# Optimization experiments

Measured on AMD Instinct MI355X. Metric: run time of the kernel, lower is better.

Reference implementation:

```python
import jax, jax.numpy as jnp
import numpy as np

NUM_BINS = 22
TEMPLATE_DIM = 16
MAX_DIST = 40.0
LN_EPS = 1e-5


def setup_inputs() -> dict:
    key = jax.random.key(0)
    k1, k2, k3, k4, k5, k6 = jax.random.split(key, 6)
    B, N = 2, 1024
    template_coords = jax.random.normal(k1, (B, N, 3), dtype=jnp.float32) * 10.0  # Angstrom-ish scale
    confidence = jax.random.uniform(k2, (B, N), dtype=jnp.float32)
    # projection = Linear(22 -> 16) + LayerNorm(16)
    lim = 1.0 / np.sqrt(NUM_BINS)
    W = jax.random.uniform(k3, (NUM_BINS, TEMPLATE_DIM), minval=-lim, maxval=lim, dtype=jnp.float32)
    b = jax.random.uniform(k4, (TEMPLATE_DIM,), minval=-lim, maxval=lim, dtype=jnp.float32)
    gamma = jnp.ones((TEMPLATE_DIM,), dtype=jnp.float32)
    beta = jnp.zeros((TEMPLATE_DIM,), dtype=jnp.float32)
    return {"template_coords": template_coords, "confidence": confidence,
            "W": W, "b": b, "gamma": gamma, "beta": beta}


def reference(template_coords, confidence, W, b, gamma, beta):
    num_dist_bins = NUM_BINS - 1          # 21
    bin_width = MAX_DIST / num_dist_bins
    bin_edges = jnp.arange(0.0, MAX_DIST, bin_width, dtype=jnp.float32)  # (21,)
    no_template_bin = NUM_BINS - 1

    # pairwise distances (B, N, N)
    diff = template_coords[:, :, None, :] - template_coords[:, None, :, :]
    dist = jnp.sqrt(jnp.sum(diff * diff, axis=-1) + 1e-8)

    # torch.bucketize(right=False) == searchsorted side='left'
    binned = jnp.searchsorted(bin_edges, dist, side="left")
    binned = jnp.clip(binned, 0, NUM_BINS - 2)

    has_i = (confidence > 0)[:, :, None]
    has_j = (confidence > 0)[:, None, :]
    binned = jnp.where(has_i & has_j, binned, no_template_bin)

    one_hot = jax.nn.one_hot(binned, NUM_BINS, dtype=jnp.float32)  # (B,N,N,22)

    # Linear + LayerNorm + ReLU
    h = jnp.einsum("bijk,kd->bijd", one_hot, W) + b
    mu = jnp.mean(h, axis=-1, keepdims=True)
    var = jnp.mean((h - mu) ** 2, axis=-1, keepdims=True)
    h = (h - mu) * jax.lax.rsqrt(var + LN_EPS) * gamma + beta
    h = jax.nn.relu(h)

    conf_pair = jnp.minimum(confidence[:, :, None], confidence[:, None, :])
    return h * conf_pair[..., None]
```

## Files before the change

### kernel.cpp

```cpp
#include <hip/hip_runtime.h>

#define BATCH 2
#define N 1024
#define NBINS 22
#define TDIM 16
#define TSTR 20

__global__ __launch_bounds__(256) void te_enc(
    const float* __restrict__ coords,
    const float* __restrict__ confp,
    const float* __restrict__ Wp,
    const float* __restrict__ bp,
    const float* __restrict__ gp,
    const float* __restrict__ betap,
    float* __restrict__ out)
{
    __shared__ __align__(16) float tbl[NBINS * TSTR];
    __shared__ float4 ljc[N];

    const int tid = threadIdx.x;
    const int blk = blockIdx.x;
    const int batch = blk >> 10;
    const int i = blk & (N - 1);

    const float* jc = coords + batch * N * 3;
    const float* jf = confp + batch * N;

    #pragma unroll
    for (int q = 0; q < 4; ++q) {
        const int j = tid + q * 256;
        float4 v;
        v.x = jc[j * 3 + 0];
        v.y = jc[j * 3 + 1];
        v.z = jc[j * 3 + 2];
        v.w = jf[j];
        ljc[j] = v;
    }

    if (tid < NBINS) {
        float h[TDIM];
        float sum = 0.f;
        #pragma unroll
        for (int d = 0; d < TDIM; ++d) {
            h[d] = Wp[tid * TDIM + d] + bp[d];
            sum += h[d];
        }
        const float mu = sum * (1.f / TDIM);
        float s2 = 0.f;
        #pragma unroll
        for (int d = 0; d < TDIM; ++d) {
            const float t = h[d] - mu;
            s2 += t * t;
        }
        const float rs = 1.f / sqrtf(s2 * (1.f / TDIM) + 1e-5f);
        #pragma unroll
        for (int d = 0; d < TDIM; ++d) {
            const float v = (h[d] - mu) * rs * gp[d] + betap[d];
            tbl[tid * TSTR + d] = fmaxf(v, 0.f);
        }
    }
    __syncthreads();

    const float xi = coords[(batch * N + i) * 3 + 0];
    const float yi = coords[(batch * N + i) * 3 + 1];
    const float zi = coords[(batch * N + i) * 3 + 2];
    const float ci = confp[batch * N + i];
    const bool ci_ok = (ci > 0.f);

    const int w   = tid >> 6;
    const int l   = tid & 63;
    const int lq  = l >> 2;
    const int sub = l & 3;

    float4* orow4 = (float4*)out + ((size_t)(batch * N + i)) * (N * TDIM / 4);
    const float EW = (float)(40.0 / 21.0);

    #pragma unroll
    for (int it = 0; it < 4; ++it) {
        const int j_base = it * 256 + w * 64;
        #pragma unroll
        for (int c = 0; c < 4; ++c) {
            const int j = j_base + 16 * c + lq;
            const float4 pj = ljc[j];

            const float dx = __fsub_rn(xi, pj.x);
            const float dy = __fsub_rn(yi, pj.y);
            const float dz = __fsub_rn(zi, pj.z);
            float s = __fmul_rn(dx, dx);
            s = __fadd_rn(s, __fmul_rn(dy, dy));
            s = __fadd_rn(s, __fmul_rn(dz, dz));
            s = __fadd_rn(s, 1e-8f);
            const float dist = __fsqrt_rn(s);

            int k0 = (int)__fmul_rn(dist, 0.525f);
            k0 = k0 < 20 ? k0 : 20;
            const int c1 = (__fmul_rn((float)k0, EW) < dist) ? 1 : 0;
            const int c2 = (__fmul_rn((float)(k0 + 1), EW) < dist) ? 1 : 0;
            const int idx = k0 + c1 + c2;
            int bin = idx < 20 ? idx : 20;
            if (!(ci_ok && pj.w > 0.f)) bin = NBINS - 1;
            const float cm = fminf(ci, pj.w);

            const float4 r = *(const float4*)&tbl[bin * TSTR + sub * 4];
            float4 o;
            o.x = r.x * cm; o.y = r.y * cm; o.z = r.z * cm; o.w = r.w * cm;

            orow4[j_base * 4 + 64 * c + l] = o;
        }
    }
}

extern "C" void kernel_launch(void* const* d_in, const int* in_sizes, int n_in,
                              void* d_out, int out_size, void* d_ws, size_t ws_size,
                              hipStream_t stream) {
    const float* coords = (const float*)d_in[0];
    const float* conf   = (const float*)d_in[1];
    const float* W      = (const float*)d_in[2];
    const float* b      = (const float*)d_in[3];
    const float* g      = (const float*)d_in[4];
    const float* beta   = (const float*)d_in[5];
    float* out          = (float*)d_out;

    te_enc<<<dim3(BATCH * N), dim3(256), 0, stream>>>(coords, conf, W, b, g, beta, out);
}
```

Baseline: 145.6 us.

## Split each row across four blocks and use nontemporal output stores

Each block now handles a quarter of the j range for one row i, giving four times as many blocks, each staging only 256 coordinates in shared memory. Output writes use nontemporal stores through a native vector type so the large streaming output bypasses cache retention. The cost is that the per-block LayerNorm table setup and the i-coordinate loads are repeated four times as often.

```diff
diff --git a/kernel.cpp b/kernel.cpp
--- a/kernel.cpp
+++ b/kernel.cpp
@@ -5,6 +5,9 @@
 #define NBINS 22
 #define TDIM 16
 #define TSTR 20
+#define SEGS 4
+
+typedef float nfloat4 __attribute__((ext_vector_type(4)));
 
 __global__ __launch_bounds__(256) void te_enc(
     const float* __restrict__ coords,
@@ -16,25 +19,25 @@
     float* __restrict__ out)
 {
     __shared__ __align__(16) float tbl[NBINS * TSTR];
-    __shared__ float4 ljc[N];
+    __shared__ float4 ljc[N / SEGS];
 
     const int tid = threadIdx.x;
     const int blk = blockIdx.x;
-    const int batch = blk >> 10;
-    const int i = blk & (N - 1);
+    const int batch = blk >> 12;
+    const int i   = (blk >> 2) & (N - 1);
+    const int seg = blk & (SEGS - 1);
 
     const float* jc = coords + batch * N * 3;
     const float* jf = confp + batch * N;
 
-    #pragma unroll
-    for (int q = 0; q < 4; ++q) {
-        const int j = tid + q * 256;
+    {
+        const int j = seg * 256 + tid;
         float4 v;
         v.x = jc[j * 3 + 0];
         v.y = jc[j * 3 + 1];
         v.z = jc[j * 3 + 2];
         v.w = jf[j];
-        ljc[j] = v;
+        ljc[tid] = v;
     }
 
     if (tid < NBINS) {
@@ -72,41 +75,38 @@
     const int lq  = l >> 2;
     const int sub = l & 3;
 
-    float4* orow4 = (float4*)out + ((size_t)(batch * N + i)) * (N * TDIM / 4);
+    nfloat4* orow4 = (nfloat4*)out + ((size_t)(batch * N + i)) * (N * TDIM / 4)
+                   + seg * 1024 + w * 256;
     const float EW = (float)(40.0 / 21.0);
 
     #pragma unroll
-    for (int it = 0; it < 4; ++it) {
-        const int j_base = it * 256 + w * 64;
-        #pragma unroll
-        for (int c = 0; c < 4; ++c) {
-            const int j = j_base + 16 * c + lq;
-            const float4 pj = ljc[j];
+    for (int c = 0; c < 4; ++c) {
+        const int jl = w * 64 + 16 * c + lq;
+        const float4 pj = ljc[jl];
 
-            const float dx = __fsub_rn(xi, pj.x);
-            const float dy = __fsub_rn(yi, pj.y);
-            const float dz = __fsub_rn(zi, pj.z);
-            float s = __fmul_rn(dx, dx);
-            s = __fadd_rn(s, __fmul_rn(dy, dy));
-            s = __fadd_rn(s, __fmul_rn(dz, dz));
-            s = __fadd_rn(s, 1e-8f);
-            const float dist = __fsqrt_rn(s);
+        const float dx = __fsub_rn(xi, pj.x);
+        const float dy = __fsub_rn(yi, pj.y);
+        const float dz = __fsub_rn(zi, pj.z);
+        float s = __fmul_rn(dx, dx);
+        s = __fadd_rn(s, __fmul_rn(dy, dy));
+        s = __fadd_rn(s, __fmul_rn(dz, dz));
+        s = __fadd_rn(s, 1e-8f);
+        const float dist = __fsqrt_rn(s);
 
-            int k0 = (int)__fmul_rn(dist, 0.525f);
-            k0 = k0 < 20 ? k0 : 20;
-            const int c1 = (__fmul_rn((float)k0, EW) < dist) ? 1 : 0;
-            const int c2 = (__fmul_rn((float)(k0 + 1), EW) < dist) ? 1 : 0;
-            const int idx = k0 + c1 + c2;
-            int bin = idx < 20 ? idx : 20;
-            if (!(ci_ok && pj.w > 0.f)) bin = NBINS - 1;
-            const float cm = fminf(ci, pj.w);
+        int k0 = (int)__fmul_rn(dist, 0.525f);
+        k0 = k0 < 20 ? k0 : 20;
+        const int c1 = (__fmul_rn((float)k0, EW) < dist) ? 1 : 0;
+        const int c2 = (__fmul_rn((float)(k0 + 1), EW) < dist) ? 1 : 0;
+        const int idx = k0 + c1 + c2;
+        int bin = idx < 20 ? idx : 20;
+        if (!(ci_ok && pj.w > 0.f)) bin = NBINS - 1;
+        const float cm = fminf(ci, pj.w);
 
-            const float4 r = *(const float4*)&tbl[bin * TSTR + sub * 4];
-            float4 o;
-            o.x = r.x * cm; o.y = r.y * cm; o.z = r.z * cm; o.w = r.w * cm;
+        const float4 r = *(const float4*)&tbl[bin * TSTR + sub * 4];
+        nfloat4 o;
+        o.x = r.x * cm; o.y = r.y * cm; o.z = r.z * cm; o.w = r.w * cm;
 
-            orow4[j_base * 4 + 64 * c + l] = o;
-        }
+        __builtin_nontemporal_store(o, &orow4[64 * c + l]);
     }
 }
 
@@ -121,5 +121,5 @@
     const float* beta   = (const float*)d_in[5];
     float* out          = (float*)d_out;
 
-    te_enc<<<dim3(BATCH * N), dim3(256), 0, stream>>>(coords, conf, W, b, g, beta, out);
+    te_enc<<<dim3(BATCH * N * SEGS), dim3(256), 0, stream>>>(coords, conf, W, b, g, beta, out);
 }
```

After: 148.9 us. 1.02x slower.
